# Performance work log

Hardware: AMD Instinct MI355X
Metric: run time of the kernel (lower is better)

The kernel has to match this reference:

```python
import jax, jax.numpy as jnp
import numpy as np


def _gru_scan(x, m, d, Wih, Whh, bih, bhh):
    # Returns pre-update hidden at each step (hiddens.append(hidden) BEFORE rnn_cell)
    H = Whh.shape[1]
    B = x.shape[0]
    h0 = jnp.zeros((B, H), x.dtype)
    xs = (jnp.swapaxes(x, 0, 1), jnp.swapaxes(m, 0, 1), jnp.swapaxes(d, 0, 1))  # [T,B,V]

    def step(h, inp):
        xt, mt, dt = inp
        gi = jnp.concatenate([xt, mt, dt], axis=1) @ Wih.T + bih  # [B,3H]
        gh = h @ Whh.T + bhh
        ir, iz, inn = jnp.split(gi, 3, axis=1)
        hr, hz, hn = jnp.split(gh, 3, axis=1)
        r = jax.nn.sigmoid(ir + hr)
        z = jax.nn.sigmoid(iz + hz)
        n = jnp.tanh(inn + r * hn)
        h_new = (1.0 - z) * n + z * h
        return h_new, h

    _, hs = jax.lax.scan(step, h0, xs)
    return jnp.swapaxes(hs, 0, 1)  # [B,T,H]


def setup_inputs() -> dict:
    key = jax.random.key(0)
    B, T, V, H = 512, 128, 59, 512
    ks = jax.random.split(key, 12)

    def u(k, shape, fan_in):
        s = 1.0 / np.sqrt(fan_in).astype(np.float32)
        return jax.random.uniform(k, shape, jnp.float32, -s, s)

    return {
        "values": jax.random.normal(ks[0], (B, T, V), jnp.float32),
        "masks": (jax.random.uniform(ks[1], (B, T, V)) < 0.8).astype(jnp.float32),
        "deltas_f": jax.random.uniform(ks[2], (B, T, V), jnp.float32),
        "deltas_b": jax.random.uniform(ks[3], (B, T, V), jnp.float32),
        # GRUCell(input=3V, hidden=H)
        "Wih": u(ks[4], (3 * H, 3 * V), 3 * V),
        "Whh": u(ks[5], (3 * H, H), H),
        "bih": jnp.zeros((3 * H,), jnp.float32),
        "bhh": jnp.zeros((3 * H,), jnp.float32),
        # hist_reg: Linear(2H -> V)
        "Wh": u(ks[6], (V, 2 * H), 2 * H),
        "bh": jnp.zeros((V,), jnp.float32),
        "Wf": u(ks[7], (V, V), V),
        "bf": jnp.zeros((V,), jnp.float32),
        # weight_combine: Linear(2V -> V)
        "Wc": u(ks[8], (V, 2 * V), 2 * V),
        "bc": jnp.zeros((V,), jnp.float32),
        # imputation: Linear(V -> V)
        "Wi": u(ks[9], (V, V), V),
        "bi": jnp.zeros((V,), jnp.float32),
    }


def reference(values, masks, deltas_f, deltas_b, Wih, Whh, bih, bhh,
              Wh, bh, Wf, bf, Wc, bc, Wi, bi):
    V = values.shape[-1]
    # forward-direction hiddens
    hf = _gru_scan(values, masks, deltas_f, Wih, Whh, bih, bhh)  # [B,T,H]
    # backward-direction: run GRU on time-flipped x/masks with deltas_b, then reverse list
    hb = _gru_scan(values[:, ::-1], masks[:, ::-1], deltas_b, Wih, Whh, bih, bhh)[:, ::-1]
    h = jnp.concatenate([hf, hb], axis=-1)  # [B,T,2H]
    x_v = h @ Wh.T + bh  # hist_reg
    mdiag = 1.0 - jnp.eye(V, dtype=values.dtype)
    x_u = values @ (Wf * mdiag).T + bf  # feat_reg
    x_h = x_u + jnp.concatenate([x_v, masks], axis=-1) @ Wc.T + bc
    imp = x_h @ Wi.T + bi
    # per-timestep masked MAE, summed over T (denominator is per-step mask count)
    num = jnp.sum(jnp.abs(values - imp) * masks, axis=(0, 2))  # [T]
    den = jnp.sum(masks, axis=(0, 2)) + 1e-5
    x_loss = jnp.sum(num / den)
    x_imp = masks * values + (1.0 - masks) * imp
    return x_imp, x_loss
```

## Files before the change

kernel.cpp:

```cpp
#include <hip/hip_runtime.h>
#include <stdint.h>


typedef unsigned short ushort_t;
typedef __bf16 bf16x8 __attribute__((ext_vector_type(8)));
typedef float f32x4 __attribute__((ext_vector_type(4)));
typedef unsigned int u32x4 __attribute__((ext_vector_type(4)));

__device__ __forceinline__ ushort_t f2bf(float f) {
    union { float f; uint32_t u; } c; c.f = f;
    uint32_t u = c.u;
    uint32_t r = (u + 0x7FFFu + ((u >> 16) & 1u)) >> 16;
    return (ushort_t)r;
}

__device__ __forceinline__ u32x4 load_b128_cached(const void* p) {
    u32x4 d;
    asm volatile("global_load_dwordx4 %0, %1, off" : "=v"(d) : "v"(p) : "memory");
    return d;
}
__device__ __forceinline__ u32x4 load_b128_mall(const void* p) {
    u32x4 d;
    asm volatile("global_load_dwordx4 %0, %1, off sc0 sc1" : "=v"(d) : "v"(p) : "memory");
    return d;
}
__device__ __forceinline__ void store_b16_mall(void* p, unsigned v) {
    asm volatile("global_store_short %0, %1, off sc0 sc1" :: "v"(p), "v"(v) : "memory");
}

__device__ __forceinline__ float fast_sigmoid(float x) {
    float e = __expf(-x);
    return __builtin_amdgcn_rcpf(1.f + e);
}
__device__ __forceinline__ float fast_tanh(float x) {
    float xc = fminf(fmaxf(x, -15.f), 15.f);
    float e = __expf(-2.f * xc);
    return (1.f - e) * __builtin_amdgcn_rcpf(1.f + e);
}

__global__ void prep_small(const float* __restrict__ Wih, const float* __restrict__ Whh,
                           const float* __restrict__ Wh,
                           const float* __restrict__ Wf, const float* __restrict__ bf_,
                           const float* __restrict__ Wc, const float* __restrict__ bc,
                           const float* __restrict__ Wi, const float* __restrict__ bi,
                           ushort_t* __restrict__ WhhB, ushort_t* __restrict__ WihB,
                           ushort_t* __restrict__ WhpB,
                           ushort_t* __restrict__ hf0, ushort_t* __restrict__ hb0,
                           float* __restrict__ hstate,
                           ushort_t* __restrict__ Wpost1, ushort_t* __restrict__ Wpost2,
                           float* __restrict__ bcP, float* __restrict__ biP,
                           unsigned* __restrict__ bar)
{
    long long gid = (long long)blockIdx.x * blockDim.x + threadIdx.x;
    long long stride = (long long)gridDim.x * blockDim.x;

    for (long long i = gid; i < 16 * 64; i += stride) bar[i] = 0u;
    for (long long i = gid; i < 1024LL * 512; i += stride) hstate[i] = 0.f;
    for (long long i = gid; i < 512LL * 512; i += stride) { hf0[i] = 0; hb0[i] = 0; }
    for (long long i = gid; i < 1536LL * 512; i += stride) WhhB[i] = f2bf(Whh[i]);
    for (long long i = gid; i < 1536LL * 192; i += stride) {
        int n = (int)(i / 192), c = (int)(i % 192);
        WihB[i] = (c < 177) ? f2bf(Wih[n * 177 + c]) : (ushort_t)0;
    }
    for (long long i = gid; i < 64LL * 1024; i += stride) {
        int n = (int)(i >> 10), k = (int)(i & 1023);
        WhpB[i] = (n < 59) ? f2bf(Wh[n * 1024 + k]) : (ushort_t)0;
    }
    for (long long i = gid; i < 64LL * 192; i += stride) {
        int n = (int)(i / 192), c = (int)(i % 192);
        float w = 0.f;
        if (n < 59) {
            if (c < 59)       w = (c == n) ? 0.f : Wf[n * 59 + c];
            else if (c < 118) w = Wc[n * 118 + (c - 59)];
            else if (c < 177) w = Wc[n * 118 + 59 + (c - 118)];
        }
        Wpost1[i] = f2bf(w);
    }
    for (long long i = gid; i < 64LL * 64; i += stride) {
        int n = (int)(i >> 6), k = (int)(i & 63);
        Wpost2[i] = (n < 59 && k < 59) ? f2bf(Wi[n * 59 + k]) : (ushort_t)0;
    }
    for (long long i = gid; i < 64; i += stride) {
        bcP[i] = (i < 59) ? (bf_[i] + bc[i]) : 0.f;
        biP[i] = (i < 59) ? bi[i] : 0.f;
    }
}

__global__ __launch_bounds__(192)
void prep_panels(const float* __restrict__ values, const float* __restrict__ masks,
                 const float* __restrict__ deltas_f, const float* __restrict__ deltas_b,
                 ushort_t* __restrict__ xcat_f, ushort_t* __restrict__ xcat_b,
                 ushort_t* __restrict__ pcat)
{
    const int row = blockIdx.x;
    const int c = threadIdx.x;
    const int b = row >> 7, t = row & 127;
    const int tr = 127 - t;
    const long long rowr = (long long)b * 128 + tr;

    float vf = 0.f;
    if (c < 59)       vf = values  [(long long)row * 59 + c];
    else if (c < 118) vf = masks   [(long long)row * 59 + (c - 59)];
    else if (c < 177) vf = deltas_f[(long long)row * 59 + (c - 118)];
    xcat_f[((size_t)t * 512 + b) * 192 + c] = (c < 177) ? f2bf(vf) : (ushort_t)0;

    float vb = 0.f;
    if (c < 59)       vb = values  [rowr * 59 + c];
    else if (c < 118) vb = masks   [rowr * 59 + (c - 59)];
    else if (c < 177) vb = deltas_b[(long long)row * 59 + (c - 118)];
    xcat_b[((size_t)t * 512 + b) * 192 + c] = (c < 177) ? f2bf(vb) : (ushort_t)0;

    if (c < 59)
        pcat[(size_t)row * 192 + c] = f2bf(values[(long long)row * 59 + c]);
    else if (c >= 118 && c < 177)
        pcat[(size_t)row * 192 + c] = f2bf(masks[(long long)row * 59 + (c - 118)]);
    else if (c >= 177)
        pcat[(size_t)row * 192 + c] = 0;
}

__global__ __launch_bounds__(512)
void recurrence_kernel(const ushort_t* __restrict__ WhhB, const ushort_t* __restrict__ WihB,
                       const float* __restrict__ bih, const float* __restrict__ bhh,
                       const ushort_t* __restrict__ xcat_f, const ushort_t* __restrict__ xcat_b,
                       ushort_t* __restrict__ hfS, ushort_t* __restrict__ hbS,
                       unsigned* __restrict__ bar)
{
    extern __shared__ char smem_c[];
    ushort_t* Bw = (ushort_t*)smem_c;
    ushort_t* As = Bw + 96 * 704;

    const int tid  = threadIdx.x;
    const int blk  = blockIdx.x;
    const int ublk = blk & 15;
    const int mblk = blk >> 4;
    const int u0   = ublk * 32;
    const bool fwd = (mblk < 8);
    const int rbase = (fwd ? mblk : mblk - 8) * 64;
    const ushort_t* xbase = fwd ? xcat_f : xcat_b;
    ushort_t* hS = fwd ? hfS : hbS;
    unsigned* gctr = bar + (unsigned)mblk * 64;

    for (int i = tid; i < 96 * 88; i += 512) {
        int row = i / 88, q = i - row * 88;
        int g = row >> 5, u = u0 + (row & 31);
        const ushort_t* src = (q < 64)
            ? WhhB + ((size_t)(g * 512 + u)) * 512 + q * 8
            : WihB + ((size_t)(g * 512 + u)) * 192 + (q - 64) * 8;
        int qs = q ^ (row & 7);
        *(u32x4*)&Bw[row * 704 + qs * 8] = *(const u32x4*)src;
    }

    const int lane = tid & 63, wv = tid >> 6;
    const int mt = wv >> 1, tc = wv & 1;
    const int l15 = lane & 15, lhi = lane >> 4;
    const int arow = tid >> 3, aj = tid & 7;
    const int awoff = arow * 64 + ((aj ^ (arow & 7)) * 8);
    const int aSw = l15 & 7;

    const int u = u0 + tc * 16 + l15;
    const float bR  = bih[u] + bhh[u];
    const float bZ  = bih[512 + u] + bhh[512 + u];
    const float bNX = bih[1024 + u];
    const float bNH = bhh[1024 + u];
    asm volatile("" :: "v"(bR), "v"(bZ), "v"(bNX), "v"(bNH));
    asm volatile("s_waitcnt vmcnt(0) lgkmcnt(0)" ::: "memory");
    __syncthreads();

    f32x4 hreg = {0.f, 0.f, 0.f, 0.f};
    f32x4 zero = {0.f, 0.f, 0.f, 0.f};
    u32x4 rx[3];
    u32x4 rh[8];
    f32x4 accR = zero, accZ = zero, accNX = zero, accNH = zero;

    auto mfma_pos = [&](int cbuf, int jBbase, f32x4& accN) {
        const ushort_t* Ab = As + cbuf * 4096;
        #pragma unroll
        for (int ks = 0; ks < 64; ks += 32) {
            int j  = (ks >> 3) + lhi;
            int jB = jBbase + j;
            bf16x8 a  = *(const bf16x8*)&Ab[(mt * 16 + l15) * 64 + ((j ^ aSw) * 8)];
            bf16x8 b0 = *(const bf16x8*)&Bw[( 0 + tc * 16 + l15) * 704 + ((jB ^ aSw) * 8)];
            bf16x8 b1 = *(const bf16x8*)&Bw[(32 + tc * 16 + l15) * 704 + ((jB ^ aSw) * 8)];
            bf16x8 b2 = *(const bf16x8*)&Bw[(64 + tc * 16 + l15) * 704 + ((jB ^ aSw) * 8)];
            accR = __builtin_amdgcn_mfma_f32_16x16x32_bf16(a, b0, accR, 0, 0, 0);
            accZ = __builtin_amdgcn_mfma_f32_16x16x32_bf16(a, b1, accZ, 0, 0, 0);
            accN = __builtin_amdgcn_mfma_f32_16x16x32_bf16(a, b2, accN, 0, 0, 0);
        }
    };

    {
        const ushort_t* xr0 = xbase + (size_t)(rbase + arow) * 192 + aj * 8;
        rx[0] = load_b128_cached(xr0);
        rx[1] = load_b128_cached(xr0 + 64);
        rx[2] = load_b128_cached(xr0 + 128);
    }
    asm volatile("s_waitcnt vmcnt(0)" ::: "memory");

    {
        const ushort_t* hrow = hS + (size_t)(rbase + arow) * 512 + aj * 8;
        #pragma unroll
        for (int j = 0; j < 8; ++j) rh[j] = load_b128_mall(hrow + j * 64);
    }

    *(u32x4*)&As[4096 + awoff] = rx[0]; __syncthreads();
    mfma_pos(1, 64, accNX);
    *(u32x4*)&As[awoff] = rx[1]; __syncthreads();
    mfma_pos(0, 72, accNX);
    *(u32x4*)&As[4096 + awoff] = rx[2]; __syncthreads();
    mfma_pos(1, 80, accNX);

#define S2_STAGE(JN, WN)                                                      \
    asm volatile("s_waitcnt vmcnt(" #WN ")" ::: "memory");                    \
    *(u32x4*)&As[((JN) & 1) * 4096 + awoff] = rh[JN];                         \
    __syncthreads();

    for (int t = 0; t < 127; ++t) {
        {
            const ushort_t* xrn = xbase + (size_t)(t + 1) * 98304
                                + (size_t)(rbase + arow) * 192 + aj * 8;
            rx[0] = load_b128_cached(xrn);
            rx[1] = load_b128_cached(xrn + 64);
            rx[2] = load_b128_cached(xrn + 128);
        }

        accNH = zero;
        S2_STAGE(0, 10) mfma_pos(0,  0, accNH);
        S2_STAGE(1,  9) mfma_pos(1,  8, accNH);
        S2_STAGE(2,  8) mfma_pos(0, 16, accNH);
        S2_STAGE(3,  7) mfma_pos(1, 24, accNH);
        S2_STAGE(4,  6) mfma_pos(0, 32, accNH);
        S2_STAGE(5,  5) mfma_pos(1, 40, accNH);
        S2_STAGE(6,  4) mfma_pos(0, 48, accNH);
        S2_STAGE(7,  3) mfma_pos(1, 56, accNH);

        ushort_t* hdst = hS + (size_t)(t + 1) * 262144;
        #pragma unroll
        for (int reg = 0; reg < 4; ++reg) {
            int m = rbase + mt * 16 + lhi * 4 + reg;
            float rr = fast_sigmoid(accR[reg] + bR);
            float zz = fast_sigmoid(accZ[reg] + bZ);
            float nn = fast_tanh(accNX[reg] + bNX + rr * (accNH[reg] + bNH));
            float hnew = (1.f - zz) * nn + zz * hreg[reg];
            hreg[reg] = hnew;
            store_b16_mall(hdst + (size_t)m * 512 + u, (unsigned)f2bf(hnew));
        }
        asm volatile("s_waitcnt vmcnt(0)" ::: "memory");
        __syncthreads();

        if (t < 126) {
            if (tid == 0) {
                atomicAdd(gctr, 1u);
                unsigned target = (unsigned)(t + 1) * 16u;
                while (__hip_atomic_load(gctr, __ATOMIC_RELAXED,
                                         __HIP_MEMORY_SCOPE_AGENT) < target)
                    __builtin_amdgcn_s_sleep(1);
            }
            __syncthreads();

            {
                const ushort_t* hrow = hS + (size_t)(t + 1) * 262144
                                     + (size_t)(rbase + arow) * 512 + aj * 8;
                #pragma unroll
                for (int j = 0; j < 8; ++j) rh[j] = load_b128_mall(hrow + j * 64);
            }

            accR = zero; accZ = zero; accNX = zero;
            *(u32x4*)&As[4096 + awoff] = rx[0]; __syncthreads();
            mfma_pos(1, 64, accNX);
            *(u32x4*)&As[awoff] = rx[1]; __syncthreads();
            mfma_pos(0, 72, accNX);
            *(u32x4*)&As[4096 + awoff] = rx[2]; __syncthreads();
            mfma_pos(1, 80, accNX);
        }
    }
#undef S2_STAGE
}

__global__ __launch_bounds__(512)
void step_kernel(const ushort_t* __restrict__ hsrcF, const ushort_t* __restrict__ hsrcB,
                 ushort_t* __restrict__ hdstF, ushort_t* __restrict__ hdstB,
                 const ushort_t* __restrict__ xF, const ushort_t* __restrict__ xB,
                 const ushort_t* __restrict__ WhhB, const ushort_t* __restrict__ WihB,
                 const float* __restrict__ bih, const float* __restrict__ bhh,
                 float* __restrict__ hstate)
{
    __shared__ __align__(16) ushort_t As[64 * 64];
    __shared__ __align__(16) ushort_t Bs[96 * 64];

    const int tid  = threadIdx.x;
    const int ublk = blockIdx.x;
    const int mblk = blockIdx.y;
    const int u0   = ublk * 32;
    const bool fwd = (mblk < 8);
    const ushort_t* hsrc = fwd ? hsrcF : hsrcB;
    const ushort_t* xsrc = fwd ? xF : xB;
    ushort_t* hdst = fwd ? hdstF : hdstB;
    const int rbase = (fwd ? mblk : mblk - 8) * 64;

    const int lane = tid & 63, wv = tid >> 6;
    const int mt = wv >> 1, tc = wv & 1;
    const int l15 = lane & 15, lhi = lane >> 4;

    f32x4 zero = {0.f, 0.f, 0.f, 0.f};
    f32x4 accR = zero, accZ = zero, accNH = zero, accNX = zero;
    const int arow = tid >> 3, ac8 = (tid & 7) * 8;

    for (int chunk = 0; chunk < 11; ++chunk) {
        const bool ph1 = (chunk < 8);
        {
            const ushort_t* src = ph1
                ? hsrc + ((size_t)(rbase + arow)) * 512 + chunk * 64 + ac8
                : xsrc + ((size_t)(rbase + arow)) * 192 + (chunk - 8) * 64 + ac8;
            *(uint4*)&As[arow * 64 + ac8] = *(const uint4*)src;
        }
        {
            int rowB = tid >> 3; int c8 = (tid & 7) * 8;
            int g = rowB >> 5; int u = u0 + (rowB & 31);
            const ushort_t* src = ph1
                ? WhhB + ((size_t)(g * 512 + u)) * 512 + chunk * 64 + c8
                : WihB + ((size_t)(g * 512 + u)) * 192 + (chunk - 8) * 64 + c8;
            *(uint4*)&Bs[rowB * 64 + c8] = *(const uint4*)src;
            if (tid < 256) {
                int u2 = tid + 512;
                rowB = u2 >> 3; c8 = (u2 & 7) * 8;
                g = rowB >> 5; u = u0 + (rowB & 31);
                src = ph1
                    ? WhhB + ((size_t)(g * 512 + u)) * 512 + chunk * 64 + c8
                    : WihB + ((size_t)(g * 512 + u)) * 192 + (chunk - 8) * 64 + c8;
                *(uint4*)&Bs[rowB * 64 + c8] = *(const uint4*)src;
            }
        }
        __syncthreads();
        #pragma unroll
        for (int ks = 0; ks < 64; ks += 32) {
            bf16x8 a  = *(const bf16x8*)&As[(mt * 16 + l15) * 64 + ks + lhi * 8];
            bf16x8 b0 = *(const bf16x8*)&Bs[( 0 + tc * 16 + l15) * 64 + ks + lhi * 8];
            bf16x8 b1 = *(const bf16x8*)&Bs[(32 + tc * 16 + l15) * 64 + ks + lhi * 8];
            bf16x8 b2 = *(const bf16x8*)&Bs[(64 + tc * 16 + l15) * 64 + ks + lhi * 8];
            accR = __builtin_amdgcn_mfma_f32_16x16x32_bf16(a, b0, accR, 0, 0, 0);
            accZ = __builtin_amdgcn_mfma_f32_16x16x32_bf16(a, b1, accZ, 0, 0, 0);
            if (ph1) accNH = __builtin_amdgcn_mfma_f32_16x16x32_bf16(a, b2, accNH, 0, 0, 0);
            else     accNX = __builtin_amdgcn_mfma_f32_16x16x32_bf16(a, b2, accNX, 0, 0, 0);
        }
        __syncthreads();
    }

    const int u = u0 + tc * 16 + l15;
    const float bR  = bih[u] + bhh[u];
    const float bZ  = bih[512 + u] + bhh[512 + u];
    const float bNX = bih[1024 + u];
    const float bNH = bhh[1024 + u];
    #pragma unroll
    for (int reg = 0; reg < 4; ++reg) {
        int m = mblk * 64 + mt * 16 + lhi * 4 + reg;
        float r = 1.f / (1.f + __expf(-(accR[reg] + bR)));
        float z = 1.f / (1.f + __expf(-(accZ[reg] + bZ)));
        float n = tanhf(accNX[reg] + bNX + r * (accNH[reg] + bNH));
        size_t idx = (size_t)m * 512 + u;
        float hold = hstate[idx];
        float hnew = (1.f - z) * n + z * hold;
        hstate[idx] = hnew;
        size_t bloc = (size_t)(fwd ? m : m - 512) * 512 + u;
        hdst[bloc] = f2bf(hnew);
    }
}

__global__ __launch_bounds__(256)
void xv_kernel(const ushort_t* __restrict__ hf, const ushort_t* __restrict__ hb,
               const ushort_t* __restrict__ WhpB, const float* __restrict__ bh,
               ushort_t* __restrict__ pcat)
{
    __shared__ __align__(16) ushort_t As[128 * 64];
    __shared__ __align__(16) ushort_t Bs[64 * 64];
    const int b = blockIdx.x;
    const int tid = threadIdx.x;
    const int lane = tid & 63, wv = tid >> 6;
    const int l15 = lane & 15, lhi = lane >> 4;

    f32x4 zero = {0.f, 0.f, 0.f, 0.f};
    f32x4 acc[2][4];
    #pragma unroll
    for (int i = 0; i < 2; ++i)
        #pragma unroll
        for (int j = 0; j < 4; ++j) acc[i][j] = zero;

    for (int chunk = 0; chunk < 16; ++chunk) {
        const bool fw = (chunk < 8);
        #pragma unroll
        for (int s = 0; s < 4; ++s) {
            int unit = tid + s * 256;
            int row = unit >> 3;
            int c8 = (unit & 7) * 8;
            const ushort_t* src = fw
                ? hf + ((size_t)row * 512 + b) * 512 + chunk * 64 + c8
                : hb + ((size_t)(127 - row) * 512 + b) * 512 + (chunk - 8) * 64 + c8;
            *(uint4*)&As[row * 64 + c8] = *(const uint4*)src;
        }
        #pragma unroll
        for (int s = 0; s < 2; ++s) {
            int unit = tid + s * 256;
            int row = unit >> 3;
            int c8 = (unit & 7) * 8;
            *(uint4*)&Bs[row * 64 + c8] =
                *(const uint4*)(WhpB + (size_t)row * 1024 + chunk * 64 + c8);
        }
        __syncthreads();
        #pragma unroll
        for (int ks = 0; ks < 64; ks += 32) {
            bf16x8 bfr[4];
            #pragma unroll
            for (int nt = 0; nt < 4; ++nt)
                bfr[nt] = *(const bf16x8*)&Bs[(nt * 16 + l15) * 64 + ks + lhi * 8];
            #pragma unroll
            for (int mt2 = 0; mt2 < 2; ++mt2) {
                bf16x8 a = *(const bf16x8*)&As[(wv * 32 + mt2 * 16 + l15) * 64 + ks + lhi * 8];
                #pragma unroll
                for (int nt = 0; nt < 4; ++nt)
                    acc[mt2][nt] = __builtin_amdgcn_mfma_f32_16x16x32_bf16(a, bfr[nt], acc[mt2][nt], 0, 0, 0);
            }
        }
        __syncthreads();
    }
    #pragma unroll
    for (int mt2 = 0; mt2 < 2; ++mt2) {
        #pragma unroll
        for (int nt = 0; nt < 4; ++nt) {
            int col = nt * 16 + l15;
            if (col < 59) {
                float bhc = bh[col];
                #pragma unroll
                for (int reg = 0; reg < 4; ++reg) {
                    int t = wv * 32 + mt2 * 16 + lhi * 4 + reg;
                    pcat[((size_t)b * 128 + t) * 192 + 59 + col] = f2bf(acc[mt2][nt][reg] + bhc);
                }
            }
        }
    }
}

__global__ __launch_bounds__(256)
void post_kernel(const ushort_t* __restrict__ pcat,
                 const ushort_t* __restrict__ Wpost1, const ushort_t* __restrict__ Wpost2,
                 const float* __restrict__ bcP, const float* __restrict__ biP,
                 const float* __restrict__ values, const float* __restrict__ masks,
                 float* __restrict__ out, float* __restrict__ pnum, float* __restrict__ pden)
{
    __shared__ __align__(16) ushort_t A1[64 * 200];
    __shared__ __align__(16) ushort_t B1[64 * 200];
    __shared__ __align__(16) ushort_t B2[64 * 72];

    const int tid = threadIdx.x;
    const int blk = blockIdx.x;
    const int lane = tid & 63, wv = tid >> 6;
    const int l15 = lane & 15, lhi = lane >> 4;

    #pragma unroll
    for (int s = 0; s < 6; ++s) {
        int unit = tid + s * 256;
        int row = unit / 24, c8 = (unit % 24) * 8;
        *(uint4*)&A1[row * 200 + c8] =
            *(const uint4*)(pcat + ((size_t)blk * 64 + row) * 192 + c8);
        *(uint4*)&B1[row * 200 + c8] =
            *(const uint4*)(Wpost1 + (size_t)row * 192 + c8);
    }
    #pragma unroll
    for (int s = 0; s < 2; ++s) {
        int unit = tid + s * 256;
        int row = unit >> 3, c8 = (unit & 7) * 8;
        *(uint4*)&B2[row * 72 + c8] = *(const uint4*)(Wpost2 + (size_t)row * 64 + c8);
    }
    __syncthreads();

    f32x4 zero = {0.f, 0.f, 0.f, 0.f};
    f32x4 acc1[4];
    #pragma unroll
    for (int nt = 0; nt < 4; ++nt) acc1[nt] = zero;

    #pragma unroll
    for (int ks = 0; ks < 192; ks += 32) {
        bf16x8 a = *(const bf16x8*)&A1[(wv * 16 + l15) * 200 + ks + lhi * 8];
        #pragma unroll
        for (int nt = 0; nt < 4; ++nt) {
            bf16x8 bb = *(const bf16x8*)&B1[(nt * 16 + l15) * 200 + ks + lhi * 8];
            acc1[nt] = __builtin_amdgcn_mfma_f32_16x16x32_bf16(a, bb, acc1[nt], 0, 0, 0);
        }
    }
    __syncthreads();

    #pragma unroll
    for (int nt = 0; nt < 4; ++nt) {
        int col = nt * 16 + l15;
        float bcv = bcP[col];
        #pragma unroll
        for (int reg = 0; reg < 4; ++reg) {
            int row = wv * 16 + lhi * 4 + reg;
            A1[row * 72 + col] = f2bf(acc1[nt][reg] + bcv);
        }
    }
    __syncthreads();

    f32x4 acc2[4];
    #pragma unroll
    for (int nt = 0; nt < 4; ++nt) acc2[nt] = zero;
    #pragma unroll
    for (int ks = 0; ks < 64; ks += 32) {
        bf16x8 a = *(const bf16x8*)&A1[(wv * 16 + l15) * 72 + ks + lhi * 8];
        #pragma unroll
        for (int nt = 0; nt < 4; ++nt) {
            bf16x8 bb = *(const bf16x8*)&B2[(nt * 16 + l15) * 72 + ks + lhi * 8];
            acc2[nt] = __builtin_amdgcn_mfma_f32_16x16x32_bf16(a, bb, acc2[nt], 0, 0, 0);
        }
    }

    float biR[4];
    #pragma unroll
    for (int nt = 0; nt < 4; ++nt) biR[nt] = biP[nt * 16 + l15];

    #pragma unroll
    for (int reg = 0; reg < 4; ++reg) {
        size_t rowg = (size_t)blk * 64 + wv * 16 + lhi * 4 + reg;
        float esum = 0.f, dsum = 0.f;
        #pragma unroll
        for (int nt = 0; nt < 4; ++nt) {
            int col = nt * 16 + l15;
            if (col < 59) {
                float imp = acc2[nt][reg] + biR[nt];
                float v = values[rowg * 59 + col];
                float m = masks [rowg * 59 + col];
                out[rowg * 59 + col] = m * v + (1.f - m) * imp;
                esum += fabsf(v - imp) * m;
                dsum += m;
            }
        }
        #pragma unroll
        for (int o = 1; o < 16; o <<= 1) {
            esum += __shfl_xor(esum, o);
            dsum += __shfl_xor(dsum, o);
        }
        if (l15 == 0) { pnum[rowg] = esum; pden[rowg] = dsum; }
    }
}

__global__ __launch_bounds__(512)
void loss_kernel(const float* __restrict__ pnum, const float* __restrict__ pden,
                 float* __restrict__ out)
{
    __shared__ float sn[512], sd[512];
    int tid = threadIdx.x;
    int t = tid & 127, q = tid >> 7;
    float a = 0.f, b = 0.f;
    for (int i = 0; i < 128; ++i) {
        int bb = q * 128 + i;
        a += pnum[(size_t)bb * 128 + t];
        b += pden[(size_t)bb * 128 + t];
    }
    sn[tid] = a; sd[tid] = b;
    __syncthreads();
    if (q == 0) {
        float A = sn[t] + sn[128 + t] + sn[256 + t] + sn[384 + t];
        float B = sd[t] + sd[128 + t] + sd[256 + t] + sd[384 + t];
        sn[t] = A / (B + 1e-5f);
    }
    __syncthreads();
    if (tid == 0) {
        float s = 0.f;
        for (int i = 0; i < 128; ++i) s += sn[i];
        out[3866624] = s;
    }
}

extern "C" void kernel_launch(void* const* d_in, const int* in_sizes, int n_in,
                              void* d_out, int out_size, void* d_ws, size_t ws_size,
                              hipStream_t stream)
{
    const float* values   = (const float*)d_in[0];
    const float* masks    = (const float*)d_in[1];
    const float* deltas_f = (const float*)d_in[2];
    const float* deltas_b = (const float*)d_in[3];
    const float* Wih = (const float*)d_in[4];
    const float* Whh = (const float*)d_in[5];
    const float* bih = (const float*)d_in[6];
    const float* bhh = (const float*)d_in[7];
    const float* Wh  = (const float*)d_in[8];
    const float* bh  = (const float*)d_in[9];
    const float* Wf  = (const float*)d_in[10];
    const float* bf_ = (const float*)d_in[11];
    const float* Wc  = (const float*)d_in[12];
    const float* bc  = (const float*)d_in[13];
    const float* Wi  = (const float*)d_in[14];
    const float* bi  = (const float*)d_in[15];
    float* out = (float*)d_out;

    uint8_t* ws = (uint8_t*)d_ws;
    size_t off = 0;
    auto alloc = [&](size_t bytes) -> void* {
        void* p = ws + off;
        off = (off + bytes + 255) & ~((size_t)255);
        return p;
    };
    ushort_t* xcat_f = (ushort_t*)alloc(128ULL * 512 * 192 * 2);
    ushort_t* xcat_b = (ushort_t*)alloc(128ULL * 512 * 192 * 2);
    ushort_t* WhhB   = (ushort_t*)alloc(1536ULL * 512 * 2);
    ushort_t* WihB   = (ushort_t*)alloc(1536ULL * 192 * 2);
    ushort_t* WhpB   = (ushort_t*)alloc(64ULL * 1024 * 2);
    ushort_t* hfS    = (ushort_t*)alloc(128ULL * 512 * 512 * 2);
    ushort_t* hbS    = (ushort_t*)alloc(128ULL * 512 * 512 * 2);
    float*    hstate = (float*)alloc(1024ULL * 512 * 4);
    ushort_t* pcat   = (ushort_t*)alloc(65536ULL * 192 * 2);
    ushort_t* Wpost1 = (ushort_t*)alloc(64ULL * 192 * 2);
    ushort_t* Wpost2 = (ushort_t*)alloc(64ULL * 64 * 2);
    float*    bcP    = (float*)alloc(64 * 4);
    float*    biP    = (float*)alloc(64 * 4);
    float*    pnum   = (float*)alloc(65536ULL * 4);
    float*    pden   = (float*)alloc(65536ULL * 4);
    unsigned* bar    = (unsigned*)alloc(16 * 64 * 4);

    prep_small<<<1024, 256, 0, stream>>>(Wih, Whh, Wh, Wf, bf_, Wc, bc, Wi, bi,
                                         WhhB, WihB, WhpB, hfS, hbS, hstate,
                                         Wpost1, Wpost2, bcP, biP, bar);
    prep_panels<<<65536, 192, 0, stream>>>(values, masks, deltas_f, deltas_b,
                                           xcat_f, xcat_b, pcat);

    const unsigned smemBytes = (96u * 704u + 2u * 64u * 64u) * 2u;
    hipError_t aerr = hipFuncSetAttribute((const void*)recurrence_kernel,
                                          hipFuncAttributeMaxDynamicSharedMemorySize,
                                          (int)smemBytes);
    hipError_t lerr = hipErrorUnknown;
    if (aerr == hipSuccess) {
        const ushort_t* a0 = WhhB; const ushort_t* a1 = WihB;
        const float* a2 = bih; const float* a3 = bhh;
        const ushort_t* a4 = xcat_f; const ushort_t* a5 = xcat_b;
        ushort_t* a6 = hfS; ushort_t* a7 = hbS;
        unsigned* a8 = bar;
        void* args[] = { &a0, &a1, &a2, &a3, &a4, &a5, &a6, &a7, &a8 };
        lerr = hipLaunchCooperativeKernel((const void*)recurrence_kernel,
                                          dim3(256), dim3(512), args, smemBytes, stream);
    }
    if (lerr != hipSuccess) {
        for (int t = 0; t < 127; ++t) {
            step_kernel<<<dim3(16, 16), 512, 0, stream>>>(
                hfS + (size_t)t * 512 * 512, hbS + (size_t)t * 512 * 512,
                hfS + (size_t)(t + 1) * 512 * 512, hbS + (size_t)(t + 1) * 512 * 512,
                xcat_f + (size_t)t * 512 * 192, xcat_b + (size_t)t * 512 * 192,
                WhhB, WihB, bih, bhh, hstate);
        }
    }

    xv_kernel<<<512, 256, 0, stream>>>(hfS, hbS, WhpB, bh, pcat);
    post_kernel<<<1024, 256, 0, stream>>>(pcat, Wpost1, Wpost2, bcP, biP,
                                          values, masks, out, pnum, pden);
    loss_kernel<<<1, 512, 0, stream>>>(pnum, pden, out);
}
```

Baseline: 877.0 us.

## Overlap hidden-state loads with input-projection MFMAs and parallelize loss reduction

The recurrence loop is reordered so each step issues the loads of the previous hidden state first, then computes the input-projection MFMAs while those loads are in flight. The remaining h chunks are streamed through a 5-register ring with staged waitcnts, which lowers register pressure and hides global-memory latency after the grid barrier. The loss reduction now runs on 128 blocks, one per timestep, with wave shuffles and an atomicAdd into an output slot that is zeroed in prep. Atomic float accumulation makes the summation order nondeterministic, and the tighter manual vmcnt ordering depends on counting outstanding loads correctly.

```diff
diff --git a/kernel.cpp b/kernel.cpp
--- a/kernel.cpp
+++ b/kernel.cpp
@@ -49,11 +49,12 @@
                            float* __restrict__ hstate,
                            ushort_t* __restrict__ Wpost1, ushort_t* __restrict__ Wpost2,
                            float* __restrict__ bcP, float* __restrict__ biP,
-                           unsigned* __restrict__ bar)
+                           unsigned* __restrict__ bar, float* __restrict__ outp)
 {
     long long gid = (long long)blockIdx.x * blockDim.x + threadIdx.x;
     long long stride = (long long)gridDim.x * blockDim.x;
 
+    if (gid == 0) outp[3866624] = 0.f;
     for (long long i = gid; i < 16 * 64; i += stride) bar[i] = 0u;
     for (long long i = gid; i < 1024LL * 512; i += stride) hstate[i] = 0.f;
     for (long long i = gid; i < 512LL * 512; i += stride) { hf0[i] = 0; hb0[i] = 0; }
@@ -169,10 +170,9 @@
     f32x4 hreg = {0.f, 0.f, 0.f, 0.f};
     f32x4 zero = {0.f, 0.f, 0.f, 0.f};
     u32x4 rx[3];
-    u32x4 rh[8];
-    f32x4 accR = zero, accZ = zero, accNX = zero, accNH = zero;
-
-    auto mfma_pos = [&](int cbuf, int jBbase, f32x4& accN) {
+    u32x4 rh[5];
+
+    auto mfma_pos = [&](int cbuf, int jBbase, f32x4& aR, f32x4& aZ, f32x4& accN) {
         const ushort_t* Ab = As + cbuf * 4096;
         #pragma unroll
         for (int ks = 0; ks < 64; ks += 32) {
@@ -182,8 +182,8 @@
             bf16x8 b0 = *(const bf16x8*)&Bw[( 0 + tc * 16 + l15) * 704 + ((jB ^ aSw) * 8)];
             bf16x8 b1 = *(const bf16x8*)&Bw[(32 + tc * 16 + l15) * 704 + ((jB ^ aSw) * 8)];
             bf16x8 b2 = *(const bf16x8*)&Bw[(64 + tc * 16 + l15) * 704 + ((jB ^ aSw) * 8)];
-            accR = __builtin_amdgcn_mfma_f32_16x16x32_bf16(a, b0, accR, 0, 0, 0);
-            accZ = __builtin_amdgcn_mfma_f32_16x16x32_bf16(a, b1, accZ, 0, 0, 0);
+            aR   = __builtin_amdgcn_mfma_f32_16x16x32_bf16(a, b0, aR, 0, 0, 0);
+            aZ   = __builtin_amdgcn_mfma_f32_16x16x32_bf16(a, b1, aZ, 0, 0, 0);
             accN = __builtin_amdgcn_mfma_f32_16x16x32_bf16(a, b2, accN, 0, 0, 0);
         }
     };
@@ -196,25 +196,27 @@
     }
     asm volatile("s_waitcnt vmcnt(0)" ::: "memory");
 
-    {
-        const ushort_t* hrow = hS + (size_t)(rbase + arow) * 512 + aj * 8;
-        #pragma unroll
-        for (int j = 0; j < 8; ++j) rh[j] = load_b128_mall(hrow + j * 64);
-    }
-
-    *(u32x4*)&As[4096 + awoff] = rx[0]; __syncthreads();
-    mfma_pos(1, 64, accNX);
-    *(u32x4*)&As[awoff] = rx[1]; __syncthreads();
-    mfma_pos(0, 72, accNX);
-    *(u32x4*)&As[4096 + awoff] = rx[2]; __syncthreads();
-    mfma_pos(1, 80, accNX);
-
-#define S2_STAGE(JN, WN)                                                      \
-    asm volatile("s_waitcnt vmcnt(" #WN ")" ::: "memory");                    \
-    *(u32x4*)&As[((JN) & 1) * 4096 + awoff] = rh[JN];                         \
-    __syncthreads();
-
     for (int t = 0; t < 127; ++t) {
+        const ushort_t* hrow = hS + (size_t)t * 262144 + (size_t)(rbase + arow) * 512 + aj * 8;
+        ushort_t* hdst = hS + (size_t)(t + 1) * 262144;
+
+        f32x4 accR = zero, accZ = zero, accNX = zero, accNH = zero;
+
+        rh[0] = load_b128_mall(hrow);
+        rh[1] = load_b128_mall(hrow + 64);
+        rh[2] = load_b128_mall(hrow + 128);
+
+        *(u32x4*)&As[awoff] = rx[0];
+        __syncthreads();
+
+        mfma_pos(0, 64, accR, accZ, accNX);
+        rh[3] = load_b128_mall(hrow + 3 * 64);
+        *(u32x4*)&As[4096 + awoff] = rx[1];
+        __syncthreads();
+
+        mfma_pos(1, 72, accR, accZ, accNX);
+        rh[4] = load_b128_mall(hrow + 4 * 64);
+        *(u32x4*)&As[awoff] = rx[2];
         {
             const ushort_t* xrn = xbase + (size_t)(t + 1) * 98304
                                 + (size_t)(rbase + arow) * 192 + aj * 8;
@@ -222,18 +224,53 @@
             rx[1] = load_b128_cached(xrn + 64);
             rx[2] = load_b128_cached(xrn + 128);
         }
-
-        accNH = zero;
-        S2_STAGE(0, 10) mfma_pos(0,  0, accNH);
-        S2_STAGE(1,  9) mfma_pos(1,  8, accNH);
-        S2_STAGE(2,  8) mfma_pos(0, 16, accNH);
-        S2_STAGE(3,  7) mfma_pos(1, 24, accNH);
-        S2_STAGE(4,  6) mfma_pos(0, 32, accNH);
-        S2_STAGE(5,  5) mfma_pos(1, 40, accNH);
-        S2_STAGE(6,  4) mfma_pos(0, 48, accNH);
-        S2_STAGE(7,  3) mfma_pos(1, 56, accNH);
-
-        ushort_t* hdst = hS + (size_t)(t + 1) * 262144;
+        __syncthreads();
+
+        mfma_pos(0, 80, accR, accZ, accNX);
+        asm volatile("s_waitcnt vmcnt(7)" ::: "memory");
+        *(u32x4*)&As[4096 + awoff] = rh[0];
+        rh[0] = load_b128_mall(hrow + 5 * 64);
+        __syncthreads();
+
+        mfma_pos(1, 0, accR, accZ, accNH);
+        asm volatile("s_waitcnt vmcnt(7)" ::: "memory");
+        *(u32x4*)&As[awoff] = rh[1];
+        rh[1] = load_b128_mall(hrow + 6 * 64);
+        __syncthreads();
+
+        mfma_pos(0, 8, accR, accZ, accNH);
+        asm volatile("s_waitcnt vmcnt(7)" ::: "memory");
+        *(u32x4*)&As[4096 + awoff] = rh[2];
+        rh[2] = load_b128_mall(hrow + 7 * 64);
+        __syncthreads();
+
+        mfma_pos(1, 16, accR, accZ, accNH);
+        asm volatile("s_waitcnt vmcnt(7)" ::: "memory");
+        *(u32x4*)&As[awoff] = rh[3];
+        __syncthreads();
+
+        mfma_pos(0, 24, accR, accZ, accNH);
+        asm volatile("s_waitcnt vmcnt(6)" ::: "memory");
+        *(u32x4*)&As[4096 + awoff] = rh[4];
+        __syncthreads();
+
+        mfma_pos(1, 32, accR, accZ, accNH);
+        asm volatile("s_waitcnt vmcnt(2)" ::: "memory");
+        *(u32x4*)&As[awoff] = rh[0];
+        __syncthreads();
+
+        mfma_pos(0, 40, accR, accZ, accNH);
+        asm volatile("s_waitcnt vmcnt(1)" ::: "memory");
+        *(u32x4*)&As[4096 + awoff] = rh[1];
+        __syncthreads();
+
+        mfma_pos(1, 48, accR, accZ, accNH);
+        asm volatile("s_waitcnt vmcnt(0)" ::: "memory");
+        *(u32x4*)&As[awoff] = rh[2];
+        __syncthreads();
+
+        mfma_pos(0, 56, accR, accZ, accNH);
+
         #pragma unroll
         for (int reg = 0; reg < 4; ++reg) {
             int m = rbase + mt * 16 + lhi * 4 + reg;
@@ -244,10 +281,10 @@
             hreg[reg] = hnew;
             store_b16_mall(hdst + (size_t)m * 512 + u, (unsigned)f2bf(hnew));
         }
-        asm volatile("s_waitcnt vmcnt(0)" ::: "memory");
-        __syncthreads();
 
         if (t < 126) {
+            asm volatile("s_waitcnt vmcnt(0)" ::: "memory");
+            __syncthreads();
             if (tid == 0) {
                 atomicAdd(gctr, 1u);
                 unsigned target = (unsigned)(t + 1) * 16u;
@@ -256,24 +293,8 @@
                     __builtin_amdgcn_s_sleep(1);
             }
             __syncthreads();
-
-            {
-                const ushort_t* hrow = hS + (size_t)(t + 1) * 262144
-                                     + (size_t)(rbase + arow) * 512 + aj * 8;
-                #pragma unroll
-                for (int j = 0; j < 8; ++j) rh[j] = load_b128_mall(hrow + j * 64);
-            }
-
-            accR = zero; accZ = zero; accNX = zero;
-            *(u32x4*)&As[4096 + awoff] = rx[0]; __syncthreads();
-            mfma_pos(1, 64, accNX);
-            *(u32x4*)&As[awoff] = rx[1]; __syncthreads();
-            mfma_pos(0, 72, accNX);
-            *(u32x4*)&As[4096 + awoff] = rx[2]; __syncthreads();
-            mfma_pos(1, 80, accNX);
-        }
-    }
-#undef S2_STAGE
+        }
+    }
 }
 
 __global__ __launch_bounds__(512)
@@ -541,31 +562,30 @@
     }
 }
 
-__global__ __launch_bounds__(512)
+__global__ __launch_bounds__(256)
 void loss_kernel(const float* __restrict__ pnum, const float* __restrict__ pden,
                  float* __restrict__ out)
 {
-    __shared__ float sn[512], sd[512];
-    int tid = threadIdx.x;
-    int t = tid & 127, q = tid >> 7;
+    __shared__ float sn[4], sd[4];
+    const int t = blockIdx.x;
+    const int tid = threadIdx.x;
     float a = 0.f, b = 0.f;
-    for (int i = 0; i < 128; ++i) {
-        int bb = q * 128 + i;
+    for (int bb = tid; bb < 512; bb += 256) {
         a += pnum[(size_t)bb * 128 + t];
         b += pden[(size_t)bb * 128 + t];
     }
-    sn[tid] = a; sd[tid] = b;
-    __syncthreads();
-    if (q == 0) {
-        float A = sn[t] + sn[128 + t] + sn[256 + t] + sn[384 + t];
-        float B = sd[t] + sd[128 + t] + sd[256 + t] + sd[384 + t];
-        sn[t] = A / (B + 1e-5f);
-    }
+    #pragma unroll
+    for (int o = 32; o >= 1; o >>= 1) {
+        a += __shfl_xor(a, o);
+        b += __shfl_xor(b, o);
+    }
+    const int wv = tid >> 6;
+    if ((tid & 63) == 0) { sn[wv] = a; sd[wv] = b; }
     __syncthreads();
     if (tid == 0) {
-        float s = 0.f;
-        for (int i = 0; i < 128; ++i) s += sn[i];
-        out[3866624] = s;
+        float A = sn[0] + sn[1] + sn[2] + sn[3];
+        float B = sd[0] + sd[1] + sd[2] + sd[3];
+        atomicAdd(out + 3866624, A / (B + 1e-5f));
     }
 }
 
@@ -617,7 +637,7 @@
 
     prep_small<<<1024, 256, 0, stream>>>(Wih, Whh, Wh, Wf, bf_, Wc, bc, Wi, bi,
                                          WhhB, WihB, WhpB, hfS, hbS, hstate,
-                                         Wpost1, Wpost2, bcP, biP, bar);
+                                         Wpost1, Wpost2, bcP, biP, bar, out);
     prep_panels<<<65536, 192, 0, stream>>>(values, masks, deltas_f, deltas_b,
                                            xcat_f, xcat_b, pcat);
 
@@ -649,5 +669,5 @@
     xv_kernel<<<512, 256, 0, stream>>>(hfS, hbS, WhpB, bh, pcat);
     post_kernel<<<1024, 256, 0, stream>>>(pcat, Wpost1, Wpost2, bcP, biP,
                                           values, masks, out, pnum, pden);
-    loss_kernel<<<1, 512, 0, stream>>>(pnum, pden, out);
-}
+    loss_kernel<<<128, 256, 0, stream>>>(pnum, pden, out);
+}
```

New measurement: 840.4 us. 1.04x faster.
